# Performance work log

Hardware: AMD Instinct MI355X
Metric: run time of the kernel (lower is better)

## Reference

```python
import jax, jax.numpy as jnp
import numpy as np

B, T, D, H = 256, 512, 512, 512


def setup_inputs() -> dict:
    key = jax.random.key(0)
    k0, k1, k2, k3 = jax.random.split(key, 4)
    sD = 1.0 / np.sqrt(D).astype(np.float32)
    sH = 1.0 / np.sqrt(H).astype(np.float32)
    return {
        "x": jax.random.normal(k0, (B, T, D), jnp.float32),
        "Wx": jax.random.normal(k1, (D, 4 * H), jnp.float32) * sD,
        "Wh": jax.random.normal(k2, (H, 4 * H), jnp.float32) * sH,
        "b": jnp.zeros((4 * H,), jnp.float32),
        "Wfc": jax.random.normal(k3, (H, 1), jnp.float32) * sH,
        "bfc": jnp.zeros((1,), jnp.float32),
    }


def reference(x, Wx, Wh, b, Wfc, bfc):
    # x: [B, T, D]. Flax LSTMCell gates (i, f, g, o):
    #   i,f,o = sigmoid(.), g = tanh(.); c' = f*c + i*g; h' = o*tanh(c')
    Bv, Tv, _ = x.shape
    Hv = Wh.shape[0]
    # Precompute all input projections in one big GEMM (same math, batched).
    xg = jnp.einsum('btd,dg->btg', x, Wx) + b  # [B, T, 4H]

    def step(carry, xt):
        c, h = carry
        gates = xt + h @ Wh                     # [B, 4H]
        i, f, g, o = jnp.split(gates, 4, axis=-1)
        c_new = jax.nn.sigmoid(f) * c + jax.nn.sigmoid(i) * jnp.tanh(g)
        h_new = jax.nn.sigmoid(o) * jnp.tanh(c_new)
        return (c_new, h_new), None

    c0 = jnp.zeros((Bv, Hv), x.dtype)
    h0 = jnp.zeros((Bv, Hv), x.dtype)
    (c_fin, h_fin), _ = jax.lax.scan(step, (c0, h0), jnp.swapaxes(xg, 0, 1))
    # fc applied to last timestep output (== final hidden state)
    return h_fin @ Wfc + bfc  # [B, 1]
```

## Files before the change

kernel.cpp:

```cpp
#include <hip/hip_runtime.h>
#include <hip/hip_bf16.h>


typedef _Float16 half8 __attribute__((ext_vector_type(8)));
typedef _Float16 half4 __attribute__((ext_vector_type(4)));
typedef int int4v __attribute__((ext_vector_type(4)));
typedef float float4v __attribute__((ext_vector_type(4)));

__device__ __forceinline__ void gl_lds16(const void* g, void* l) {
  __builtin_amdgcn_global_load_lds(
      (const __attribute__((address_space(1))) unsigned int*)g,
      (__attribute__((address_space(3))) unsigned int*)l, 16, 0, 0);
}

__device__ __forceinline__ float sigm(float v) { return 1.f / (1.f + __expf(-v)); }
__device__ __forceinline__ float tanh_(float v) { return 1.f - 2.f / (__expf(2.f * v) + 1.f); }

__global__ __launch_bounds__(256) void k_prep(
    const float* __restrict__ x, const float* __restrict__ b,
    _Float16* __restrict__ xf, float* __restrict__ bp)
{
  const long NX8 = 67108864L / 8;
  const long TOT = NX8 + 2048;
  long stride = (long)gridDim.x * blockDim.x;
  for (long id = (long)blockIdx.x * blockDim.x + threadIdx.x; id < TOT; id += stride) {
    if (id < NX8) {
      const float4v* p = (const float4v*)x + id * 2;
      float4v a = p[0], c = p[1];
      half8 o;
      o[0]=(_Float16)a[0]; o[1]=(_Float16)a[1]; o[2]=(_Float16)a[2]; o[3]=(_Float16)a[3];
      o[4]=(_Float16)c[0]; o[5]=(_Float16)c[1]; o[6]=(_Float16)c[2]; o[7]=(_Float16)c[3];
      ((half8*)xf)[id] = o;
    } else {
      int np = (int)(id - NX8);
      int j = np >> 2, gt = np & 3;
      bp[np] = b[gt * 512 + j];
    }
  }
}

__global__ __launch_bounds__(256) void k_wtr(
    const float* __restrict__ W, _Float16* __restrict__ Wt)
{
  __shared__ float lds[64][65];
  const int bbk = blockIdx.x;
  const int kt = bbk & 7, nt = bbk >> 3;
  const int tx = threadIdx.x & 63, ty = threadIdx.x >> 6;
  #pragma unroll
  for (int r = 0; r < 16; ++r) {
    int kl = ty * 16 + r;
    lds[kl][tx] = W[(long)(kt * 64 + kl) * 2048 + nt * 64 + tx];
  }
  __syncthreads();
  #pragma unroll
  for (int r = 0; r < 16; ++r) {
    int nl = ty * 16 + r;
    int n = nt * 64 + nl;
    int j = n & 511, gt = n >> 9;
    int np = j * 4 + gt;
    Wt[(long)np * 512 + kt * 64 + tx] = (_Float16)lds[tx][nl];
  }
}

__global__ __launch_bounds__(256, 2) void k_gemm_xg(
    const _Float16* __restrict__ xf, const _Float16* __restrict__ wxt,
    const float* __restrict__ bp, _Float16* __restrict__ xg)
{
  __shared__ _Float16 As[128 * 32];
  __shared__ _Float16 Bs[128 * 32];
  const int tid = threadIdx.x;
  const int w = tid >> 6, l = tid & 63;
  const int mt = blockIdx.x >> 4, nt = blockIdx.x & 15;
  const int qr = (w >> 1) * 64, qc = (w & 1) * 64;
  float4v acc[4][4];
  #pragma unroll
  for (int i = 0; i < 4; ++i)
    #pragma unroll
    for (int j = 0; j < 4; ++j) acc[i][j] = (float4v){0.f, 0.f, 0.f, 0.f};
  const int lr = l >> 2, lc = (l & 3) * 8;
  for (int kt = 0; kt < 16; ++kt) {
    __syncthreads();
    #pragma unroll
    for (int i = 0; i < 2; ++i) {
      int chunk = i * 4 + w;
      gl_lds16(xf + ((long)(mt * 128 + chunk * 16 + lr)) * 512 + kt * 32 + lc, As + chunk * 512);
      gl_lds16(wxt + ((long)(nt * 128 + chunk * 16 + lr)) * 512 + kt * 32 + lc, Bs + chunk * 512);
    }
    __syncthreads();
    half8 af[4], bf[4];
    #pragma unroll
    for (int mi = 0; mi < 4; ++mi)
      af[mi] = *(const half8*)(As + (qr + mi * 16 + (l & 15)) * 32 + (l >> 4) * 8);
    #pragma unroll
    for (int ni = 0; ni < 4; ++ni)
      bf[ni] = *(const half8*)(Bs + (qc + ni * 16 + (l & 15)) * 32 + (l >> 4) * 8);
    #pragma unroll
    for (int mi = 0; mi < 4; ++mi)
      #pragma unroll
      for (int ni = 0; ni < 4; ++ni)
        acc[mi][ni] = __builtin_amdgcn_mfma_f32_16x16x32_f16(af[mi], bf[ni], acc[mi][ni], 0, 0, 0);
  }
  #pragma unroll
  for (int ni = 0; ni < 4; ++ni) {
    int col = nt * 128 + qc + ni * 16 + (l & 15);
    float bias = bp[col];
    #pragma unroll
    for (int mi = 0; mi < 4; ++mi) {
      long R0 = (long)mt * 128 + qr + mi * 16 + (l >> 4) * 4;
      #pragma unroll
      for (int r = 0; r < 4; ++r)
        xg[(R0 + r) * 2048 + col] = (_Float16)(acc[mi][ni][r] + bias);
    }
  }
}

__global__ __launch_bounds__(256, 1) void k_scan(
    const _Float16* __restrict__ xg, const _Float16* __restrict__ wht,
    const float* __restrict__ wfc, const float* __restrict__ bfc,
    _Float16* __restrict__ hsl, unsigned int* __restrict__ flags,
    float* __restrict__ out)
{
  __shared__ unsigned int wctr;
  const int tid = threadIdx.x;
  if (tid == 0) wctr = 0;
  __syncthreads();

  const int w = tid >> 6, l = tid & 63;
  const int q = l >> 4;
  const int m = l & 15;
  const int bb = blockIdx.x;
  const int slot = bb >> 3;
  const int g = (bb & 7) * 2 + (slot >> 4);
  const int s = slot & 15;

  int4v bw0[16], bw1[16];
  {
    const _Float16* b0 = wht + ((long)(s * 128 + (2 * w + 0) * 16 + m)) * 512 + q * 8;
    const _Float16* b1 = wht + ((long)(s * 128 + (2 * w + 1) * 16 + m)) * 512 + q * 8;
    #pragma unroll
    for (int kk = 0; kk < 16; ++kk) {
      bw0[kk] = *(const int4v*)(b0 + kk * 32);
      bw1[kk] = *(const int4v*)(b1 + kk * 32);
    }
    #pragma unroll
    for (int kk = 0; kk < 16; ++kk)
      asm volatile("" : "+v"(bw0[kk]), "+v"(bw1[kk]));
  }

  float c0 = 0.f, c1 = 0.f;
  const int j0 = s * 32 + 8 * w + q;
  const int j1 = s * 32 + 8 * w + 4 + q;
  const float wf0 = wfc[j0], wf1 = wfc[j1];
  unsigned int* fl = flags + g * 256;
  const _Float16* xgr = xg + ((long)(g * 16 + m)) * 512 * 2048 + s * 128 + q * 4;
  const _Float16* hrg = hsl + (long)g * 8192 + q * 128 + m * 8;
  _Float16* hw = hsl + (long)(g * 16 + s) * 512 + w * 128 + m * 8;

  half4 xc0 = *(const half4*)(xgr + (2 * w + 0) * 16);
  half4 xc1 = *(const half4*)(xgr + (2 * w + 1) * 16);

  for (int t = 0; t < 512; ++t) {
    const int pr = t & 1;
    const long tn = (t < 511) ? (long)(t + 1) : 511L;
    const half4 xn0 = *(const half4*)(xgr + tn * 2048 + (2 * w + 0) * 16);
    const half4 xn1 = *(const half4*)(xgr + tn * 2048 + (2 * w + 1) * 16);
    if (t) {
      if (w == 0 && l < 16 && l != s) {
        unsigned int* p = fl + l * 16;
        unsigned int a = __hip_atomic_load(p, __ATOMIC_RELAXED, __HIP_MEMORY_SCOPE_AGENT);
        if (a < (unsigned)t) {
          unsigned int bq = __hip_atomic_load(p, __ATOMIC_RELAXED, __HIP_MEMORY_SCOPE_AGENT);
          unsigned int cq = __hip_atomic_load(p, __ATOMIC_RELAXED, __HIP_MEMORY_SCOPE_AGENT);
          while (a < (unsigned)t) {
            __builtin_amdgcn_s_sleep(4);
            a = bq; bq = cq;
            cq = __hip_atomic_load(p, __ATOMIC_RELAXED, __HIP_MEMORY_SCOPE_AGENT);
          }
        }
      }
      asm volatile("" ::: "memory");
      __syncthreads();
    }
    const _Float16* hr = hrg + pr * 131072;
    int4v av[16];
    #pragma unroll
    for (int kk = 0; kk < 16; ++kk)
      asm volatile("global_load_dwordx4 %0, %1, off sc0 sc1"
                   : "=&v"(av[kk]) : "v"(hr + kk * 512) : "memory");
    asm volatile("s_waitcnt vmcnt(0)" ::: "memory");
    __builtin_amdgcn_sched_barrier(0);

    float4v a0 = (float4v){0.f,0.f,0.f,0.f}, a1 = a0, b0v = a0, b1v = a0;
    #pragma unroll
    for (int kk = 0; kk < 8; ++kk) {
      a0 = __builtin_amdgcn_mfma_f32_16x16x32_f16(__builtin_bit_cast(half8, bw0[kk]),
                                                  __builtin_bit_cast(half8, av[kk]), a0, 0, 0, 0);
      a1 = __builtin_amdgcn_mfma_f32_16x16x32_f16(__builtin_bit_cast(half8, bw1[kk]),
                                                  __builtin_bit_cast(half8, av[kk]), a1, 0, 0, 0);
    }
    #pragma unroll
    for (int kk = 8; kk < 16; ++kk) {
      b0v = __builtin_amdgcn_mfma_f32_16x16x32_f16(__builtin_bit_cast(half8, bw0[kk]),
                                                   __builtin_bit_cast(half8, av[kk]), b0v, 0, 0, 0);
      b1v = __builtin_amdgcn_mfma_f32_16x16x32_f16(__builtin_bit_cast(half8, bw1[kk]),
                                                   __builtin_bit_cast(half8, av[kk]), b1v, 0, 0, 0);
    }
    a0 += b0v; a1 += b1v;
    float i0 = sigm(a0[0] + (float)xc0[0]);
    float f0 = sigm(a0[1] + (float)xc0[1]);
    float g0 = tanh_(a0[2] + (float)xc0[2]);
    float o0 = sigm(a0[3] + (float)xc0[3]);
    c0 = f0 * c0 + i0 * g0;
    float h0v = o0 * tanh_(c0);
    float i1 = sigm(a1[0] + (float)xc1[0]);
    float f1 = sigm(a1[1] + (float)xc1[1]);
    float g1 = tanh_(a1[2] + (float)xc1[2]);
    float o1 = sigm(a1[3] + (float)xc1[3]);
    c1 = f1 * c1 + i1 * g1;
    float h1v = o1 * tanh_(c1);
    unsigned int hb0 = (unsigned int)__builtin_bit_cast(unsigned short, (_Float16)h0v);
    unsigned int hb1 = (unsigned int)__builtin_bit_cast(unsigned short, (_Float16)h1v);
    unsigned int pb0 = __shfl_xor(hb0, 16);
    unsigned int pb1 = __shfl_xor(hb1, 16);
    unsigned int pair0 = hb0 | (pb0 << 16);
    unsigned int pair1 = hb1 | (pb1 << 16);
    unsigned int x0 = __shfl_xor(pair0, 32);
    unsigned int x1 = __shfl_xor(pair1, 32);
    if (q == 0) {
      int4v pk = {(int)pair0, (int)x0, (int)pair1, (int)x1};
      _Float16* dst = hw + (pr ^ 1) * 131072;
      asm volatile("global_store_dwordx4 %0, %1, off sc0 sc1"
                   :: "v"(dst), "v"(pk) : "memory");
    }
    if (t == 511) {
      float part = h0v * wf0 + h1v * wf1;
      part += __shfl_xor(part, 16);
      part += __shfl_xor(part, 32);
      if (l < 16) {
        float v = part;
        if (s == 0 && w == 0) v += bfc[0];
        atomicAdd(out + g * 16 + l, v);
      }
    } else {
      asm volatile("s_waitcnt vmcnt(0)" ::: "memory");
      if (l == 0) {
        unsigned int old = atomicAdd(&wctr, 1u);
        if (old == 4u * (unsigned)t + 3u)
          __hip_atomic_store(fl + s * 16, (unsigned)(t + 1),
                             __ATOMIC_RELAXED, __HIP_MEMORY_SCOPE_AGENT);
      }
    }
    xc0 = xn0; xc1 = xn1;
  }
}

extern "C" void kernel_launch(void* const* d_in, const int* in_sizes, int n_in,
                              void* d_out, int out_size, void* d_ws, size_t ws_size,
                              hipStream_t stream)
{
  const float* x   = (const float*)d_in[0];
  const float* Wx  = (const float*)d_in[1];
  const float* Wh  = (const float*)d_in[2];
  const float* b   = (const float*)d_in[3];
  const float* Wfc = (const float*)d_in[4];
  const float* bfc = (const float*)d_in[5];
  char* ws = (char*)d_ws;

  const size_t OFF_XG  = 0;
  const size_t OFF_XB  = 536870912UL;
  const size_t OFF_WXT = OFF_XB + 134217728UL;
  const size_t OFF_WHT = OFF_WXT + 2097152UL;
  const size_t OFF_BP  = OFF_WHT + 2097152UL;
  const size_t OFF_H   = OFF_BP + 8192UL;
  const size_t OFF_FL  = OFF_H + 524288UL;
  const size_t NEED    = OFF_FL + 16384UL;
  if (ws_size < NEED) return;

  _Float16* xgp = (_Float16*)(ws + OFF_XG);
  _Float16* xfp = (_Float16*)(ws + OFF_XB);
  _Float16* wxt = (_Float16*)(ws + OFF_WXT);
  _Float16* wht = (_Float16*)(ws + OFF_WHT);
  float*    bp  = (float*)(ws + OFF_BP);
  _Float16* hsl = (_Float16*)(ws + OFF_H);
  unsigned int* flg = (unsigned int*)(ws + OFF_FL);
  float* outp = (float*)d_out;

  hipMemsetAsync(ws + OFF_H, 0, 262144, stream);
  hipMemsetAsync(ws + OFF_FL, 0, 16384, stream);
  hipMemsetAsync(d_out, 0, sizeof(float) * 256, stream);

  k_prep<<<2048, 256, 0, stream>>>(x, b, xfp, bp);
  k_wtr<<<256, 256, 0, stream>>>(Wx, wxt);
  k_wtr<<<256, 256, 0, stream>>>(Wh, wht);
  k_gemm_xg<<<16384, 256, 0, stream>>>(xfp, wxt, bp, xgp);

  const _Float16* xgc = xgp;
  const _Float16* whtc = wht;
  void* args[] = { (void*)&xgc, (void*)&whtc, (void*)&Wfc, (void*)&bfc,
                   (void*)&hsl, (void*)&flg, (void*)&outp };
  hipLaunchCooperativeKernel((void*)k_scan, dim3(256), dim3(256), args, 0, stream);
}
```

Measured before the change: 1.881 ms.

## Fuse input-projection GEMM into the recurrent scan kernel, computing next step's gates

Drops the separate large x·Wx GEMM that wrote a big fp16 gate tensor. Instead, each scan block computes its slice of the input projection for step t+1 right after publishing h for step t, reading x and Wx directly. The goal is to remove the heavy intermediate tensor write and read, and to hide the input projection in the slack of the serial recurrence. The cost is extra MFMA work and memory traffic inside the latency-critical loop, since Wx is re-read every step. The spin-wait also drops its s_sleep backoff and becomes a tight poll, and the old path is kept as a fallback if the cooperative launch fails.

Result: slower. 4.505 ms (+139.5%).

```diff
diff --git a/kernel.cpp b/kernel.cpp
--- a/kernel.cpp
+++ b/kernel.cpp
@@ -114,7 +114,159 @@
   }
 }
 
-__global__ __launch_bounds__(256, 1) void k_scan(
+__global__ __launch_bounds__(256, 1) void k_scanf(
+    const _Float16* __restrict__ xf, const _Float16* __restrict__ wht,
+    const _Float16* __restrict__ wxt, const float* __restrict__ bp,
+    const float* __restrict__ wfc, const float* __restrict__ bfc,
+    _Float16* __restrict__ hsl, unsigned int* __restrict__ flags,
+    float* __restrict__ out)
+{
+  __shared__ unsigned int wctr;
+  const int tid = threadIdx.x;
+  if (tid == 0) wctr = 0;
+  __syncthreads();
+
+  const int w = tid >> 6, l = tid & 63;
+  const int q = l >> 4;
+  const int m = l & 15;
+  const int bb = blockIdx.x;
+  const int slot = bb >> 3;
+  const int g = (bb & 7) * 2 + (slot >> 4);
+  const int s = slot & 15;
+
+  int4v bw0[16], bw1[16];
+  {
+    const _Float16* b0 = wht + ((long)(s * 128 + (2 * w + 0) * 16 + m)) * 512 + q * 8;
+    const _Float16* b1 = wht + ((long)(s * 128 + (2 * w + 1) * 16 + m)) * 512 + q * 8;
+    #pragma unroll
+    for (int kk = 0; kk < 16; ++kk) {
+      bw0[kk] = *(const int4v*)(b0 + kk * 32);
+      bw1[kk] = *(const int4v*)(b1 + kk * 32);
+    }
+    #pragma unroll
+    for (int kk = 0; kk < 16; ++kk)
+      asm volatile("" : "+v"(bw0[kk]), "+v"(bw1[kk]));
+  }
+  const _Float16* wxp0 = wxt + ((long)(s * 128 + (2 * w + 0) * 16 + m)) * 512 + q * 8;
+  const _Float16* wxp1 = wxt + ((long)(s * 128 + (2 * w + 1) * 16 + m)) * 512 + q * 8;
+
+  float c0 = 0.f, c1 = 0.f;
+  const int j0 = s * 32 + 8 * w + q;
+  const int j1 = s * 32 + 8 * w + 4 + q;
+  const float wf0 = wfc[j0], wf1 = wfc[j1];
+  const float4v bq0 = *(const float4v*)(bp + j0 * 4);
+  const float4v bq1 = *(const float4v*)(bp + j1 * 4);
+  unsigned int* fl = flags + g * 256;
+  const _Float16* xrow = xf + ((long)(g * 16 + m)) * 512 * 512 + q * 8;
+  const _Float16* hrg = hsl + (long)g * 8192 + q * 128 + m * 8;
+  _Float16* hw = hsl + (long)(g * 16 + s) * 512 + w * 128 + m * 8;
+
+  float4v xga0 = (float4v){0.f,0.f,0.f,0.f}, xga1 = xga0;
+  #pragma unroll
+  for (int kk = 0; kk < 16; ++kk) {
+    int4v xv = *(const int4v*)(xrow + kk * 32);
+    half8 wa0 = *(const half8*)(wxp0 + kk * 32);
+    half8 wa1 = *(const half8*)(wxp1 + kk * 32);
+    xga0 = __builtin_amdgcn_mfma_f32_16x16x32_f16(wa0, __builtin_bit_cast(half8, xv), xga0, 0, 0, 0);
+    xga1 = __builtin_amdgcn_mfma_f32_16x16x32_f16(wa1, __builtin_bit_cast(half8, xv), xga1, 0, 0, 0);
+  }
+
+  for (int t = 0; t < 512; ++t) {
+    const int pr = t & 1;
+    if (t) {
+      if (w == 0 && l < 16 && l != s) {
+        unsigned int* p = fl + l * 16;
+        while (__hip_atomic_load(p, __ATOMIC_RELAXED, __HIP_MEMORY_SCOPE_AGENT)
+               < (unsigned)t) {}
+      }
+      asm volatile("" ::: "memory");
+      __syncthreads();
+    }
+    const _Float16* hr = hrg + pr * 131072;
+    half8 af[16];
+    #pragma unroll
+    for (int kk = 0; kk < 16; ++kk) {
+      union { half8 v; unsigned long long u[2]; } A;
+      A.u[0] = __hip_atomic_load((const unsigned long long*)(hr + kk * 512),
+                                 __ATOMIC_RELAXED, __HIP_MEMORY_SCOPE_AGENT);
+      A.u[1] = __hip_atomic_load((const unsigned long long*)(hr + kk * 512) + 1,
+                                 __ATOMIC_RELAXED, __HIP_MEMORY_SCOPE_AGENT);
+      af[kk] = A.v;
+    }
+    float4v a0 = xga0, a1 = xga1;
+    float4v b0v = (float4v){0.f,0.f,0.f,0.f}, b1v = b0v;
+    #pragma unroll
+    for (int kk = 0; kk < 8; ++kk) {
+      a0 = __builtin_amdgcn_mfma_f32_16x16x32_f16(__builtin_bit_cast(half8, bw0[kk]), af[kk], a0, 0, 0, 0);
+      a1 = __builtin_amdgcn_mfma_f32_16x16x32_f16(__builtin_bit_cast(half8, bw1[kk]), af[kk], a1, 0, 0, 0);
+    }
+    #pragma unroll
+    for (int kk = 8; kk < 16; ++kk) {
+      b0v = __builtin_amdgcn_mfma_f32_16x16x32_f16(__builtin_bit_cast(half8, bw0[kk]), af[kk], b0v, 0, 0, 0);
+      b1v = __builtin_amdgcn_mfma_f32_16x16x32_f16(__builtin_bit_cast(half8, bw1[kk]), af[kk], b1v, 0, 0, 0);
+    }
+    a0 += b0v; a1 += b1v;
+    float i0 = sigm(a0[0] + bq0[0]);
+    float f0 = sigm(a0[1] + bq0[1]);
+    float g0 = tanh_(a0[2] + bq0[2]);
+    float o0 = sigm(a0[3] + bq0[3]);
+    c0 = f0 * c0 + i0 * g0;
+    float h0v = o0 * tanh_(c0);
+    float i1 = sigm(a1[0] + bq1[0]);
+    float f1 = sigm(a1[1] + bq1[1]);
+    float g1 = tanh_(a1[2] + bq1[2]);
+    float o1 = sigm(a1[3] + bq1[3]);
+    c1 = f1 * c1 + i1 * g1;
+    float h1v = o1 * tanh_(c1);
+    unsigned int hb0 = (unsigned int)__builtin_bit_cast(unsigned short, (_Float16)h0v);
+    unsigned int hb1 = (unsigned int)__builtin_bit_cast(unsigned short, (_Float16)h1v);
+    unsigned int pb0 = __shfl_xor(hb0, 16);
+    unsigned int pb1 = __shfl_xor(hb1, 16);
+    unsigned int pair0 = hb0 | (pb0 << 16);
+    unsigned int pair1 = hb1 | (pb1 << 16);
+    unsigned int x0 = __shfl_xor(pair0, 32);
+    unsigned int x1 = __shfl_xor(pair1, 32);
+    if (q == 0) {
+      int4v pk = {(int)pair0, (int)x0, (int)pair1, (int)x1};
+      _Float16* dst = hw + (pr ^ 1) * 131072;
+      asm volatile("global_store_dwordx4 %0, %1, off sc0 sc1"
+                   :: "v"(dst), "v"(pk) : "memory");
+    }
+    if (t == 511) {
+      float part = h0v * wf0 + h1v * wf1;
+      part += __shfl_xor(part, 16);
+      part += __shfl_xor(part, 32);
+      if (l < 16) {
+        float v = part;
+        if (s == 0 && w == 0) v += bfc[0];
+        atomicAdd(out + g * 16 + l, v);
+      }
+    } else {
+      asm volatile("s_waitcnt vmcnt(0)" ::: "memory");
+      if (l == 0) {
+        unsigned int old = atomicAdd(&wctr, 1u);
+        if (old == 4u * (unsigned)t + 3u)
+          __hip_atomic_store(fl + s * 16, (unsigned)(t + 1),
+                             __ATOMIC_RELAXED, __HIP_MEMORY_SCOPE_AGENT);
+      }
+    }
+    if (t < 511) {
+      const _Float16* xr = xrow + (long)(t + 1) * 512;
+      float4v n0 = (float4v){0.f,0.f,0.f,0.f}, n1 = n0;
+      #pragma unroll
+      for (int kk = 0; kk < 16; ++kk) {
+        int4v xv = *(const int4v*)(xr + kk * 32);
+        half8 wa0 = *(const half8*)(wxp0 + kk * 32);
+        half8 wa1 = *(const half8*)(wxp1 + kk * 32);
+        n0 = __builtin_amdgcn_mfma_f32_16x16x32_f16(wa0, __builtin_bit_cast(half8, xv), n0, 0, 0, 0);
+        n1 = __builtin_amdgcn_mfma_f32_16x16x32_f16(wa1, __builtin_bit_cast(half8, xv), n1, 0, 0, 0);
+      }
+      xga0 = n0; xga1 = n1;
+    }
+  }
+}
+
+__global__ __launch_bounds__(256, 1) void k_scan4(
     const _Float16* __restrict__ xg, const _Float16* __restrict__ wht,
     const float* __restrict__ wfc, const float* __restrict__ bfc,
     _Float16* __restrict__ hsl, unsigned int* __restrict__ flags,
@@ -167,16 +319,8 @@
     if (t) {
       if (w == 0 && l < 16 && l != s) {
         unsigned int* p = fl + l * 16;
-        unsigned int a = __hip_atomic_load(p, __ATOMIC_RELAXED, __HIP_MEMORY_SCOPE_AGENT);
-        if (a < (unsigned)t) {
-          unsigned int bq = __hip_atomic_load(p, __ATOMIC_RELAXED, __HIP_MEMORY_SCOPE_AGENT);
-          unsigned int cq = __hip_atomic_load(p, __ATOMIC_RELAXED, __HIP_MEMORY_SCOPE_AGENT);
-          while (a < (unsigned)t) {
-            __builtin_amdgcn_s_sleep(4);
-            a = bq; bq = cq;
-            cq = __hip_atomic_load(p, __ATOMIC_RELAXED, __HIP_MEMORY_SCOPE_AGENT);
-          }
-        }
+        while (__hip_atomic_load(p, __ATOMIC_RELAXED, __HIP_MEMORY_SCOPE_AGENT)
+               < (unsigned)t) {}
       }
       asm volatile("" ::: "memory");
       __syncthreads();
@@ -292,11 +436,21 @@
   k_prep<<<2048, 256, 0, stream>>>(x, b, xfp, bp);
   k_wtr<<<256, 256, 0, stream>>>(Wx, wxt);
   k_wtr<<<256, 256, 0, stream>>>(Wh, wht);
-  k_gemm_xg<<<16384, 256, 0, stream>>>(xfp, wxt, bp, xgp);
-
-  const _Float16* xgc = xgp;
+
+  const _Float16* xfc = xfp;
   const _Float16* whtc = wht;
-  void* args[] = { (void*)&xgc, (void*)&whtc, (void*)&Wfc, (void*)&bfc,
-                   (void*)&hsl, (void*)&flg, (void*)&outp };
-  hipLaunchCooperativeKernel((void*)k_scan, dim3(256), dim3(256), args, 0, stream);
-}
+  const _Float16* wxtc = wxt;
+  const float* bpc = bp;
+  void* argsF[] = { (void*)&xfc, (void*)&whtc, (void*)&wxtc, (void*)&bpc,
+                    (void*)&Wfc, (void*)&bfc, (void*)&hsl, (void*)&flg, (void*)&outp };
+  hipError_t rc = hipLaunchCooperativeKernel((void*)k_scanf, dim3(256), dim3(256),
+                                             argsF, 0, stream);
+  if (rc != hipSuccess) {
+    (void)hipGetLastError();
+    k_gemm_xg<<<16384, 256, 0, stream>>>(xfp, wxt, bp, xgp);
+    const _Float16* xgc = xgp;
+    void* args4[] = { (void*)&xgc, (void*)&whtc, (void*)&Wfc, (void*)&bfc,
+                      (void*)&hsl, (void*)&flg, (void*)&outp };
+    hipLaunchCooperativeKernel((void*)k_scan4, dim3(256), dim3(256), args4, 0, stream);
+  }
+}
```

## Share hidden-state loads across warps via LDS and simplify flag spin-wait

Applied to the files above, without the earlier changes.

Each of the four warps now fetches a quarter of the 16 hidden-state chunks from global memory with atomic relaxed loads and stores them into shared memory. After a block barrier, every warp reads all 16 chunks from LDS for its MFMAs. Previously every warp loaded all 16 chunks itself with cache-bypassing loads. This cuts redundant global traffic per step by four, at the cost of an extra __syncthreads and an LDS round trip on the serial recurrence path. The flag poll also drops its sleep and pipelined reads in favour of a tight spin loop.

New measurement: 2.120 ms. 1.13x slower.

```diff
diff --git a/kernel.cpp b/kernel.cpp
--- a/kernel.cpp
+++ b/kernel.cpp
@@ -120,6 +120,7 @@
     _Float16* __restrict__ hsl, unsigned int* __restrict__ flags,
     float* __restrict__ out)
 {
+  __shared__ _Float16 lh[8192];
   __shared__ unsigned int wctr;
   const int tid = threadIdx.x;
   if (tid == 0) wctr = 0;
@@ -155,6 +156,7 @@
   const _Float16* xgr = xg + ((long)(g * 16 + m)) * 512 * 2048 + s * 128 + q * 4;
   const _Float16* hrg = hsl + (long)g * 8192 + q * 128 + m * 8;
   _Float16* hw = hsl + (long)(g * 16 + s) * 512 + w * 128 + m * 8;
+  const int lidx = q * 128 + m * 8;
 
   half4 xc0 = *(const half4*)(xgr + (2 * w + 0) * 16);
   half4 xc1 = *(const half4*)(xgr + (2 * w + 1) * 16);
@@ -167,43 +169,37 @@
     if (t) {
       if (w == 0 && l < 16 && l != s) {
         unsigned int* p = fl + l * 16;
-        unsigned int a = __hip_atomic_load(p, __ATOMIC_RELAXED, __HIP_MEMORY_SCOPE_AGENT);
-        if (a < (unsigned)t) {
-          unsigned int bq = __hip_atomic_load(p, __ATOMIC_RELAXED, __HIP_MEMORY_SCOPE_AGENT);
-          unsigned int cq = __hip_atomic_load(p, __ATOMIC_RELAXED, __HIP_MEMORY_SCOPE_AGENT);
-          while (a < (unsigned)t) {
-            __builtin_amdgcn_s_sleep(4);
-            a = bq; bq = cq;
-            cq = __hip_atomic_load(p, __ATOMIC_RELAXED, __HIP_MEMORY_SCOPE_AGENT);
-          }
-        }
+        while (__hip_atomic_load(p, __ATOMIC_RELAXED, __HIP_MEMORY_SCOPE_AGENT)
+               < (unsigned)t) {}
       }
       asm volatile("" ::: "memory");
       __syncthreads();
     }
     const _Float16* hr = hrg + pr * 131072;
-    int4v av[16];
-    #pragma unroll
-    for (int kk = 0; kk < 16; ++kk)
-      asm volatile("global_load_dwordx4 %0, %1, off sc0 sc1"
-                   : "=&v"(av[kk]) : "v"(hr + kk * 512) : "memory");
-    asm volatile("s_waitcnt vmcnt(0)" ::: "memory");
-    __builtin_amdgcn_sched_barrier(0);
+    #pragma unroll
+    for (int kq = 0; kq < 4; ++kq) {
+      const int kk = w * 4 + kq;
+      union { half8 v; unsigned long long u[2]; } A;
+      A.u[0] = __hip_atomic_load((const unsigned long long*)(hr + kk * 512),
+                                 __ATOMIC_RELAXED, __HIP_MEMORY_SCOPE_AGENT);
+      A.u[1] = __hip_atomic_load((const unsigned long long*)(hr + kk * 512) + 1,
+                                 __ATOMIC_RELAXED, __HIP_MEMORY_SCOPE_AGENT);
+      *(half8*)&lh[kk * 512 + lidx] = A.v;
+    }
+    __syncthreads();
 
     float4v a0 = (float4v){0.f,0.f,0.f,0.f}, a1 = a0, b0v = a0, b1v = a0;
     #pragma unroll
     for (int kk = 0; kk < 8; ++kk) {
-      a0 = __builtin_amdgcn_mfma_f32_16x16x32_f16(__builtin_bit_cast(half8, bw0[kk]),
-                                                  __builtin_bit_cast(half8, av[kk]), a0, 0, 0, 0);
-      a1 = __builtin_amdgcn_mfma_f32_16x16x32_f16(__builtin_bit_cast(half8, bw1[kk]),
-                                                  __builtin_bit_cast(half8, av[kk]), a1, 0, 0, 0);
+      half8 af = *(const half8*)&lh[kk * 512 + lidx];
+      a0 = __builtin_amdgcn_mfma_f32_16x16x32_f16(__builtin_bit_cast(half8, bw0[kk]), af, a0, 0, 0, 0);
+      a1 = __builtin_amdgcn_mfma_f32_16x16x32_f16(__builtin_bit_cast(half8, bw1[kk]), af, a1, 0, 0, 0);
     }
     #pragma unroll
     for (int kk = 8; kk < 16; ++kk) {
-      b0v = __builtin_amdgcn_mfma_f32_16x16x32_f16(__builtin_bit_cast(half8, bw0[kk]),
-                                                   __builtin_bit_cast(half8, av[kk]), b0v, 0, 0, 0);
-      b1v = __builtin_amdgcn_mfma_f32_16x16x32_f16(__builtin_bit_cast(half8, bw1[kk]),
-                                                   __builtin_bit_cast(half8, av[kk]), b1v, 0, 0, 0);
+      half8 af = *(const half8*)&lh[kk * 512 + lidx];
+      b0v = __builtin_amdgcn_mfma_f32_16x16x32_f16(__builtin_bit_cast(half8, bw0[kk]), af, b0v, 0, 0, 0);
+      b1v = __builtin_amdgcn_mfma_f32_16x16x32_f16(__builtin_bit_cast(half8, bw1[kk]), af, b1v, 0, 0, 0);
     }
     a0 += b0v; a1 += b1v;
     float i0 = sigm(a0[0] + (float)xc0[0]);
```
